# Optimization experiments

Measured on AMD Instinct MI355X. Metric: run time of the kernel, lower is better.

Reference implementation:

```python
import jax, jax.numpy as jnp
import numpy as np

B, S, H = 16, 4096, 1024   # batch, seq_len, hidden_dim
NSEG = 512                  # max segments (distinct output_mask ids) per example


def setup_inputs() -> dict:
    key = jax.random.key(0)
    k1, k2 = jax.random.split(key)
    hidden_states = jax.random.normal(k1, (B, S, H), dtype=jnp.float32)
    # non-decreasing segment ids per row, as the original loop requires
    output_mask = jnp.sort(jax.random.randint(k2, (B, S), 0, NSEG), axis=-1)
    return {"hidden_states": hidden_states, "output_mask": output_mask}


def reference(hidden_states, output_mask):
    # Fused equivalent of the per-token Python loop: mean-pool tokens sharing
    # the same (batch, segment_id) group; tokens with id == -1 are dropped.
    b, s, h = hidden_states.shape
    valid = output_mask >= 0                                     # [B, S]
    batch_idx = jnp.arange(b, dtype=output_mask.dtype)[:, None]  # [B, 1]
    # global segment id; invalid tokens routed to a dummy trailing bucket
    gid = jnp.where(valid, batch_idx * NSEG + output_mask, b * NSEG)
    gid_flat = gid.reshape(-1)                                   # [B*S]
    x = hidden_states.reshape(-1, h)                             # [B*S, H]
    sums = jax.ops.segment_sum(x, gid_flat, num_segments=b * NSEG + 1)[:-1]
    ones = jnp.ones((b * s,), dtype=hidden_states.dtype)
    counts = jax.ops.segment_sum(ones, gid_flat, num_segments=b * NSEG + 1)[:-1]
    # segment mean; empty segments yield zeros (fixed-shape analogue of torch.cat)
    return sums / jnp.maximum(counts, 1.0)[:, None]              # [B*NSEG, H]
```

## Files before the change

### kernel.cpp

```cpp
#include <hip/hip_runtime.h>

constexpr int B    = 16;
constexpr int S    = 4096;
constexpr int H    = 1024;
constexpr int NSEG = 512;

__global__ __launch_bounds__(256) void seg_mean_kernel(
    const float* __restrict__ hs,
    const int*   __restrict__ mask,
    float*       __restrict__ out)
{
    const int gid = blockIdx.x;
    const int b   = gid >> 9;
    const int seg = gid & (NSEG - 1);

    __shared__ int s_start, s_end;
    if (threadIdx.x == 0) {
        const int* row = mask + b * S;
        int lo = 0, hi = S;
        while (lo < hi) {
            int mid = (lo + hi) >> 1;
            if (row[mid] < seg) lo = mid + 1; else hi = mid;
        }
        int start = lo;
        hi = S;
        while (lo < hi) {
            int mid = (lo + hi) >> 1;
            if (row[mid] < seg + 1) lo = mid + 1; else hi = mid;
        }
        s_start = start;
        s_end   = lo;
    }
    __syncthreads();

    const int start = s_start;
    const int cnt   = s_end - start;

    const int col = threadIdx.x << 2;
    float4 acc = make_float4(0.f, 0.f, 0.f, 0.f);

    const float* base = hs + ((size_t)b * S + (size_t)start) * H + col;
    for (int t = 0; t < cnt; ++t) {
        float4 v = *reinterpret_cast<const float4*>(base + (size_t)t * H);
        acc.x += v.x; acc.y += v.y; acc.z += v.z; acc.w += v.w;
    }

    const float inv = (cnt > 0) ? (1.0f / (float)cnt) : 0.0f;
    acc.x *= inv; acc.y *= inv; acc.z *= inv; acc.w *= inv;

    *reinterpret_cast<float4*>(out + (size_t)gid * H + col) = acc;
}

extern "C" void kernel_launch(void* const* d_in, const int* in_sizes, int n_in,
                              void* d_out, int out_size, void* d_ws, size_t ws_size,
                              hipStream_t stream) {
    const float* hs   = (const float*)d_in[0];
    const int*   mask = (const int*)  d_in[1];

    float* out = (float*)d_out;

    dim3 grid(B * NSEG);
    dim3 block(256);
    seg_mean_kernel<<<grid, block, 0, stream>>>(hs, mask, out);
}
```

Baseline: 58.79 us.

## Precompute segment boundaries in separate kernel and unroll accumulation loop

```diff
diff --git a/kernel.cpp b/kernel.cpp
--- a/kernel.cpp
+++ b/kernel.cpp
@@ -5,50 +5,72 @@
 constexpr int H    = 1024;
 constexpr int NSEG = 512;
 
+__global__ __launch_bounds__(256) void seg_bounds_kernel(
+    const int* __restrict__ mask,
+    int*       __restrict__ bounds)
+{
+    const int idx = blockIdx.x * blockDim.x + threadIdx.x;
+    const int b = idx >> 12;
+    const int i = idx & (S - 1);
+
+    const int* row  = mask + b * S;
+    int*       brow = bounds + b * (NSEG + 1);
+
+    int cur  = row[i];
+    int prev = (i == 0) ? -1 : row[i - 1];
+
+    if (cur  > NSEG - 1) cur  = NSEG - 1;
+    if (prev < -1)       prev = -1;
+
+    for (int s = prev + 1; s <= cur; ++s) brow[s] = i;
+    if (i == S - 1) {
+        for (int s = (cur < 0 ? 0 : cur + 1); s <= NSEG; ++s) brow[s] = S;
+    }
+}
+
 __global__ __launch_bounds__(256) void seg_mean_kernel(
     const float* __restrict__ hs,
-    const int*   __restrict__ mask,
+    const int*   __restrict__ bounds,
     float*       __restrict__ out)
 {
     const int gid = blockIdx.x;
     const int b   = gid >> 9;
     const int seg = gid & (NSEG - 1);
 
-    __shared__ int s_start, s_end;
-    if (threadIdx.x == 0) {
-        const int* row = mask + b * S;
-        int lo = 0, hi = S;
-        while (lo < hi) {
-            int mid = (lo + hi) >> 1;
-            if (row[mid] < seg) lo = mid + 1; else hi = mid;
-        }
-        int start = lo;
-        hi = S;
-        while (lo < hi) {
-            int mid = (lo + hi) >> 1;
-            if (row[mid] < seg + 1) lo = mid + 1; else hi = mid;
-        }
-        s_start = start;
-        s_end   = lo;
-    }
-    __syncthreads();
-
-    const int start = s_start;
-    const int cnt   = s_end - start;
+    const int* brow  = bounds + b * (NSEG + 1);
+    const int  start = brow[seg];
+    const int  end   = brow[seg + 1];
+    const int  cnt   = end - start;
 
     const int col = threadIdx.x << 2;
-    float4 acc = make_float4(0.f, 0.f, 0.f, 0.f);
 
     const float* base = hs + ((size_t)b * S + (size_t)start) * H + col;
-    for (int t = 0; t < cnt; ++t) {
+
+    float4 a0 = make_float4(0.f, 0.f, 0.f, 0.f);
+    float4 a1 = make_float4(0.f, 0.f, 0.f, 0.f);
+
+    int t = 0;
+    for (; t + 4 <= cnt; t += 4) {
+        float4 v0 = *reinterpret_cast<const float4*>(base + (size_t)(t + 0) * H);
+        float4 v1 = *reinterpret_cast<const float4*>(base + (size_t)(t + 1) * H);
+        float4 v2 = *reinterpret_cast<const float4*>(base + (size_t)(t + 2) * H);
+        float4 v3 = *reinterpret_cast<const float4*>(base + (size_t)(t + 3) * H);
+        a0.x += v0.x; a0.y += v0.y; a0.z += v0.z; a0.w += v0.w;
+        a1.x += v1.x; a1.y += v1.y; a1.z += v1.z; a1.w += v1.w;
+        a0.x += v2.x; a0.y += v2.y; a0.z += v2.z; a0.w += v2.w;
+        a1.x += v3.x; a1.y += v3.y; a1.z += v3.z; a1.w += v3.w;
+    }
+    for (; t < cnt; ++t) {
         float4 v = *reinterpret_cast<const float4*>(base + (size_t)t * H);
-        acc.x += v.x; acc.y += v.y; acc.z += v.z; acc.w += v.w;
+        a0.x += v.x; a0.y += v.y; a0.z += v.z; a0.w += v.w;
     }
 
+    a0.x += a1.x; a0.y += a1.y; a0.z += a1.z; a0.w += a1.w;
+
     const float inv = (cnt > 0) ? (1.0f / (float)cnt) : 0.0f;
-    acc.x *= inv; acc.y *= inv; acc.z *= inv; acc.w *= inv;
+    a0.x *= inv; a0.y *= inv; a0.z *= inv; a0.w *= inv;
 
-    *reinterpret_cast<float4*>(out + (size_t)gid * H + col) = acc;
+    *reinterpret_cast<float4*>(out + (size_t)gid * H + col) = a0;
 }
 
 extern "C" void kernel_launch(void* const* d_in, const int* in_sizes, int n_in,
@@ -57,9 +79,9 @@
     const float* hs   = (const float*)d_in[0];
     const int*   mask = (const int*)  d_in[1];
 
-    float* out = (float*)d_out;
+    float* out    = (float*)d_out;
+    int*   bounds = (int*)d_ws;
 
-    dim3 grid(B * NSEG);
-    dim3 block(256);
-    seg_mean_kernel<<<grid, block, 0, stream>>>(hs, mask, out);
+    seg_bounds_kernel<<<dim3((B * S) / 256), dim3(256), 0, stream>>>(mask, bounds);
+    seg_mean_kernel <<<dim3(B * NSEG),       dim3(256), 0, stream>>>(hs, bounds, out);
 }
```

After: 56.33 us. -4.2%, faster.
